# Kernel tuning notes

Hardware: AMD Instinct MI355X
Metric: run time of the kernel (lower is better)

The kernel has to match this reference:

```python
import jax, jax.numpy as jnp
import numpy as np

HIDDEN = 1024
HEADS = 16
HEAD = HIDDEN // HEADS


def setup_inputs() -> dict:
    key = jax.random.key(0)
    ks = jax.random.split(key, 10)
    s = 1.0 / np.sqrt(HIDDEN)
    inp = {
        "x": jax.random.normal(ks[0], (2, 2048, HIDDEN), dtype=jnp.float32),
        "Wq": jax.random.uniform(ks[1], (HIDDEN, HIDDEN), jnp.float32, -s, s),
        "bq": jnp.zeros((HIDDEN,), jnp.float32),
        "Wk": jax.random.uniform(ks[2], (HIDDEN, HIDDEN), jnp.float32, -s, s),
        "bk": jnp.zeros((HIDDEN,), jnp.float32),
        "Wv": jax.random.uniform(ks[3], (HIDDEN, HIDDEN), jnp.float32, -s, s),
        "bv": jnp.zeros((HIDDEN,), jnp.float32),
        "Wo": jax.random.uniform(ks[4], (HIDDEN, HIDDEN), jnp.float32, -s, s),
        "bo": jnp.zeros((HIDDEN,), jnp.float32),
        "ln_g": jnp.ones((HIDDEN,), jnp.float32),
        "ln_b": jnp.zeros((HIDDEN,), jnp.float32),
    }
    return inp


def reference(x, Wq, bq, Wk, bk, Wv, bv, Wo, bo, ln_g, ln_b):
    B, S, H = x.shape
    # pre-LN (eps=1e-5 like torch LayerNorm)
    mu = jnp.mean(x, axis=-1, keepdims=True)
    var = jnp.mean(jnp.square(x - mu), axis=-1, keepdims=True)
    xn = (x - mu) * jax.lax.rsqrt(var + 1e-5) * ln_g + ln_b
    # QKV projections (torch Linear: x @ W.T + b) -> [B,S,heads,head]
    q = (xn @ Wq.T + bq).reshape(B, S, HEADS, HEAD)
    k = (xn @ Wk.T + bk).reshape(B, S, HEADS, HEAD)
    v = (xn @ Wv.T + bv).reshape(B, S, HEADS, HEAD)
    # scaled dot-product attention, naive full scores [B,heads,S,S]
    scores = jnp.einsum("bqhd,bkhd->bhqk", q, k) / jnp.sqrt(jnp.float32(HEAD))
    attn = jax.nn.softmax(scores, axis=-1)
    ctx = jnp.einsum("bhqk,bkhd->bqhd", attn, v).reshape(B, S, H)
    out = ctx @ Wo.T + bo
    return x + out  # dropout is identity in eval
```

## Files before the change

kernel.cpp:

```cpp
#include <hip/hip_runtime.h>
#include <hip/hip_bf16.h>
#include <stdint.h>

#define HID 1024
#define SEQ 2048
#define BATCH 2
#define NHEADS 16
#define HEADDIM 64
#define MROWS (BATCH*SEQ)

#define GAS __attribute__((address_space(1)))
#define LAS __attribute__((address_space(3)))

typedef __attribute__((ext_vector_type(8))) __bf16 bf16x8;
typedef __attribute__((ext_vector_type(4))) float f32x4;

__device__ __forceinline__ ushort f2bf(float f) {
  union { float f; uint32_t u; } v; v.f = f;
  return (ushort)((v.u + 0x7FFFu + ((v.u >> 16) & 1u)) >> 16);
}

__device__ __forceinline__ void gl_lds16(const void* g, void* l) {
  __builtin_amdgcn_global_load_lds((const GAS void*)g, (LAS void*)l, 16, 0, 0);
}

__global__ __launch_bounds__(256) void k_cvt(const float* __restrict__ Wq,
                                             const float* __restrict__ Wk,
                                             const float* __restrict__ Wv,
                                             const float* __restrict__ Wo,
                                             ushort* __restrict__ dst) {
  int mat = blockIdx.y;
  const float* src = (mat == 0) ? Wq : (mat == 1) ? Wk : (mat == 2) ? Wv : Wo;
  int off = (blockIdx.x * 256 + threadIdx.x) * 4;
  float4 v = *(const float4*)(src + off);
  ushort4 o;
  o.x = f2bf(v.x); o.y = f2bf(v.y); o.z = f2bf(v.z); o.w = f2bf(v.w);
  *(ushort4*)(dst + (size_t)mat * (HID * HID) + off) = o;
}

__global__ __launch_bounds__(256) void k_ln(const float* __restrict__ x,
                                            const float* __restrict__ g,
                                            const float* __restrict__ b,
                                            ushort* __restrict__ xn) {
  int row = blockIdx.x;
  int t = threadIdx.x;
  const float* xr = x + (size_t)row * HID;
  float4 v = *(const float4*)(xr + t * 4);
  float s = v.x + v.y + v.z + v.w;
  float s2 = v.x * v.x + v.y * v.y + v.z * v.z + v.w * v.w;
  for (int m = 1; m < 64; m <<= 1) { s += __shfl_xor(s, m); s2 += __shfl_xor(s2, m); }
  __shared__ float ws[4], ws2[4];
  int wid = t >> 6;
  if ((t & 63) == 0) { ws[wid] = s; ws2[wid] = s2; }
  __syncthreads();
  s = ws[0] + ws[1] + ws[2] + ws[3];
  s2 = ws2[0] + ws2[1] + ws2[2] + ws2[3];
  float mu = s * (1.0f / HID);
  float var = s2 * (1.0f / HID) - mu * mu;
  float rstd = rsqrtf(var + 1e-5f);
  float4 gg = *(const float4*)(g + t * 4);
  float4 bb = *(const float4*)(b + t * 4);
  ushort4 o;
  o.x = f2bf((v.x - mu) * rstd * gg.x + bb.x);
  o.y = f2bf((v.y - mu) * rstd * gg.y + bb.y);
  o.z = f2bf((v.z - mu) * rstd * gg.z + bb.z);
  o.w = f2bf((v.w - mu) * rstd * gg.w + bb.w);
  *(ushort4*)(xn + (size_t)row * HID + t * 4) = o;
}

__global__ __launch_bounds__(256) void k_qkv(const ushort* __restrict__ xn,
                                             const ushort* __restrict__ wmat,
                                             const float* __restrict__ bq,
                                             const float* __restrict__ bk,
                                             const float* __restrict__ bv,
                                             ushort* __restrict__ qo,
                                             ushort* __restrict__ ko,
                                             ushort* __restrict__ vo) {
  __shared__ ushort As[128 * 32];
  __shared__ ushort Bs[128 * 32];
  int tid = threadIdx.x;
  int lane = tid & 63;
  int wv = tid >> 6;
  int quad = lane >> 4;
  int l16 = lane & 15;
  int m0 = blockIdx.x * 128;
  int ng = blockIdx.y * 128;
  int mat = ng >> 10;
  int nloc = ng & 1023;
  const ushort* wptr = wmat + (size_t)mat * (HID * HID) + (size_t)nloc * HID;
  const float* bias = (mat == 0) ? bq : (mat == 1) ? bk : bv;
  ushort* outp = (mat == 0) ? qo : (mat == 1) ? ko : vo;
  const float scl = (mat == 0) ? 0.18033688011112042f : 1.0f;

  int arow = tid >> 2;
  int acol = (tid & 3) * 8;
  int wm = (wv >> 1) * 64, wn = (wv & 1) * 64;

  f32x4 acc[4][4] = {};
  for (int k0 = 0; k0 < HID; k0 += 32) {
    __syncthreads();
    for (int t = 0; t < 2; t++) {
      gl_lds16(xn + (size_t)(m0 + t * 64 + arow) * HID + k0 + acol,
               As + t * 2048 + wv * 512);
      gl_lds16(wptr + (size_t)(t * 64 + arow) * HID + k0 + acol,
               Bs + t * 2048 + wv * 512);
    }
    __syncthreads();
    bf16x8 af[4], bfr[4];
    for (int i = 0; i < 4; i++)
      af[i] = *(const bf16x8*)&As[(wm + i * 16 + l16) * 32 + quad * 8];
    for (int n = 0; n < 4; n++)
      bfr[n] = *(const bf16x8*)&Bs[(wn + n * 16 + l16) * 32 + quad * 8];
    for (int i = 0; i < 4; i++)
      for (int n = 0; n < 4; n++)
        acc[i][n] = __builtin_amdgcn_mfma_f32_16x16x32_bf16(af[i], bfr[n], acc[i][n], 0, 0, 0);
  }
  float bv4[4];
  for (int n = 0; n < 4; n++) bv4[n] = bias[nloc + wn + n * 16 + l16];
  for (int i = 0; i < 4; i++) {
    int mrow = m0 + wm + i * 16 + quad * 4;
    for (int n = 0; n < 4; n++) {
      int col = nloc + wn + n * 16 + l16;
      int h = col >> 6, d = col & 63;
      for (int r = 0; r < 4; r++) {
        int m = mrow + r;
        int bidx = m >> 11, sidx = m & 2047;
        size_t dst = (((size_t)(bidx * NHEADS + h) * SEQ) + sidx) * HEADDIM + d;
        outp[dst] = f2bf((acc[i][n][r] + bv4[n]) * scl);
      }
    }
  }
}

__global__ __launch_bounds__(256, 2) void k_attn(const ushort* __restrict__ Q,
                                                 const ushort* __restrict__ K,
                                                 const ushort* __restrict__ V,
                                                 ushort* __restrict__ ctx) {
  __shared__ ushort Ksm[64 * 72];
  __shared__ ushort Vsm[64 * 72];
  __shared__ ushort Psm[4 * 32 * 72];
  int tid = threadIdx.x, lane = tid & 63, wv = tid >> 6, quad = lane >> 4, l16 = lane & 15;
  int bh = blockIdx.y;
  int q0 = blockIdx.x * 128;
  const ushort* Qb = Q + ((size_t)bh * SEQ + q0 + wv * 32) * HEADDIM;
  const ushort* Kb = K + (size_t)bh * SEQ * HEADDIM;
  const ushort* Vb = V + (size_t)bh * SEQ * HEADDIM;
  ushort* Pw = Psm + wv * 32 * 72;

  bf16x8 qf[2][2];
  for (int m = 0; m < 2; m++)
    for (int c = 0; c < 2; c++)
      qf[m][c] = *(const bf16x8*)(Qb + (size_t)(m * 16 + l16) * HEADDIM + c * 32 + quad * 8);

  bf16x8 ones;
  for (int j = 0; j < 8; j++) ones[j] = (__bf16)1.0f;

  f32x4 Oa[2][4] = {};
  f32x4 Os[2] = {};

  for (int kt = 0; kt < SEQ / 64; kt++) {
    const ushort* Kt = Kb + (size_t)kt * 64 * HEADDIM;
    const ushort* Vt = Vb + (size_t)kt * 64 * HEADDIM;
    __syncthreads();
    for (int it = 0; it < 2; it++) {
      int u = tid + it * 256;
      int key = u >> 3, c8 = (u & 7) * 8;
      *(int4*)&Ksm[key * 72 + c8] = *(const int4*)(Kt + key * HEADDIM + c8);
      int vkey = u & 63, vd = (u >> 6) * 8;
      int4 vvv = *(const int4*)(Vt + vkey * HEADDIM + vd);
      ushort* vp = (ushort*)&vvv;
      for (int j = 0; j < 8; j++) Vsm[(vd + j) * 72 + vkey] = vp[j];
    }
    __syncthreads();

    f32x4 sacc[2][4] = {};
    for (int nt = 0; nt < 4; nt++) {
      int krow = 2 * l16 + (nt & 1) + 32 * (nt >> 1);
      for (int c = 0; c < 2; c++) {
        bf16x8 kf = *(const bf16x8*)&Ksm[krow * 72 + c * 32 + quad * 8];
        sacc[0][nt] = __builtin_amdgcn_mfma_f32_16x16x32_bf16(qf[0][c], kf, sacc[0][nt], 0, 0, 0);
        sacc[1][nt] = __builtin_amdgcn_mfma_f32_16x16x32_bf16(qf[1][c], kf, sacc[1][nt], 0, 0, 0);
      }
    }

    for (int m = 0; m < 2; m++) {
      for (int r = 0; r < 4; r++) {
        union { float f; uint32_t u; } p0, p1, p2, p3;
        p0.f = __builtin_amdgcn_exp2f(fminf(sacc[m][0][r], 80.f));
        p1.f = __builtin_amdgcn_exp2f(fminf(sacc[m][1][r], 80.f));
        p2.f = __builtin_amdgcn_exp2f(fminf(sacc[m][2][r], 80.f));
        p3.f = __builtin_amdgcn_exp2f(fminf(sacc[m][3][r], 80.f));
        uint32_t pk01 = __builtin_amdgcn_perm(p1.u, p0.u, 0x07060302u);
        uint32_t pk23 = __builtin_amdgcn_perm(p3.u, p2.u, 0x07060302u);
        int row = m * 16 + quad * 4 + r;
        *(uint32_t*)&Pw[row * 72 + 2 * l16] = pk01;
        *(uint32_t*)&Pw[row * 72 + 32 + 2 * l16] = pk23;
      }
    }

    for (int c = 0; c < 2; c++) {
      bf16x8 pf0 = *(const bf16x8*)&Pw[(l16) * 72 + c * 32 + quad * 8];
      bf16x8 pf1 = *(const bf16x8*)&Pw[(16 + l16) * 72 + c * 32 + quad * 8];
      Os[0] = __builtin_amdgcn_mfma_f32_16x16x32_bf16(pf0, ones, Os[0], 0, 0, 0);
      Os[1] = __builtin_amdgcn_mfma_f32_16x16x32_bf16(pf1, ones, Os[1], 0, 0, 0);
      for (int nt = 0; nt < 4; nt++) {
        bf16x8 vf = *(const bf16x8*)&Vsm[(nt * 16 + l16) * 72 + c * 32 + quad * 8];
        Oa[0][nt] = __builtin_amdgcn_mfma_f32_16x16x32_bf16(pf0, vf, Oa[0][nt], 0, 0, 0);
        Oa[1][nt] = __builtin_amdgcn_mfma_f32_16x16x32_bf16(pf1, vf, Oa[1][nt], 0, 0, 0);
      }
    }
  }

  int bidx = bh >> 4, h = bh & 15;
  for (int m = 0; m < 2; m++) {
    for (int r = 0; r < 4; r++) {
      float inv = 1.0f / Os[m][r];
      int sidx = q0 + wv * 32 + m * 16 + quad * 4 + r;
      size_t base = ((size_t)(bidx * SEQ) + sidx) * HID + h * HEADDIM;
      for (int nt = 0; nt < 4; nt++)
        ctx[base + nt * 16 + l16] = f2bf(Oa[m][nt][r] * inv);
    }
  }
}

__global__ __launch_bounds__(256) void k_oproj(const ushort* __restrict__ ctx,
                                               const ushort* __restrict__ wmat,
                                               const float* __restrict__ bo,
                                               const float* __restrict__ x,
                                               float* __restrict__ out) {
  __shared__ ushort As[128 * 32];
  __shared__ ushort Bs[128 * 32];
  int tid = threadIdx.x;
  int lane = tid & 63;
  int wv = tid >> 6;
  int quad = lane >> 4;
  int l16 = lane & 15;
  int m0 = blockIdx.x * 128;
  int n0 = blockIdx.y * 128;
  const ushort* wptr = wmat + (size_t)3 * (HID * HID) + (size_t)n0 * HID;
  int arow = tid >> 2;
  int acol = (tid & 3) * 8;
  int wm = (wv >> 1) * 64, wn = (wv & 1) * 64;

  f32x4 acc[4][4] = {};
  for (int k0 = 0; k0 < HID; k0 += 32) {
    __syncthreads();
    for (int t = 0; t < 2; t++) {
      gl_lds16(ctx + (size_t)(m0 + t * 64 + arow) * HID + k0 + acol,
               As + t * 2048 + wv * 512);
      gl_lds16(wptr + (size_t)(t * 64 + arow) * HID + k0 + acol,
               Bs + t * 2048 + wv * 512);
    }
    __syncthreads();
    bf16x8 af[4], bfr[4];
    for (int i = 0; i < 4; i++)
      af[i] = *(const bf16x8*)&As[(wm + i * 16 + l16) * 32 + quad * 8];
    for (int n = 0; n < 4; n++)
      bfr[n] = *(const bf16x8*)&Bs[(wn + n * 16 + l16) * 32 + quad * 8];
    for (int i = 0; i < 4; i++)
      for (int n = 0; n < 4; n++)
        acc[i][n] = __builtin_amdgcn_mfma_f32_16x16x32_bf16(af[i], bfr[n], acc[i][n], 0, 0, 0);
  }
  float bv4[4];
  for (int n = 0; n < 4; n++) bv4[n] = bo[n0 + wn + n * 16 + l16];
  for (int i = 0; i < 4; i++) {
    int mrow = m0 + wm + i * 16 + quad * 4;
    for (int n = 0; n < 4; n++) {
      int col = n0 + wn + n * 16 + l16;
      for (int r = 0; r < 4; r++) {
        size_t idx = (size_t)(mrow + r) * HID + col;
        out[idx] = acc[i][n][r] + bv4[n] + x[idx];
      }
    }
  }
}

extern "C" void kernel_launch(void* const* d_in, const int* in_sizes, int n_in,
                              void* d_out, int out_size, void* d_ws, size_t ws_size,
                              hipStream_t stream) {
  const float* x    = (const float*)d_in[0];
  const float* Wq   = (const float*)d_in[1];
  const float* bq   = (const float*)d_in[2];
  const float* Wk   = (const float*)d_in[3];
  const float* bk   = (const float*)d_in[4];
  const float* Wv   = (const float*)d_in[5];
  const float* bv   = (const float*)d_in[6];
  const float* Wo   = (const float*)d_in[7];
  const float* bo   = (const float*)d_in[8];
  const float* ln_g = (const float*)d_in[9];
  const float* ln_b = (const float*)d_in[10];
  float* out = (float*)d_out;

  const size_t MB = 1024 * 1024;
  ushort* ws_w = (ushort*)d_ws;
  ushort* xn   = (ushort*)((char*)d_ws + 8 * MB);
  ushort* Qw   = (ushort*)((char*)d_ws + 16 * MB);
  ushort* Kw   = (ushort*)((char*)d_ws + 24 * MB);
  ushort* Vw   = (ushort*)((char*)d_ws + 32 * MB);
  ushort* Cw   = (ushort*)((char*)d_ws + 40 * MB);

  k_cvt<<<dim3(1024, 4), 256, 0, stream>>>(Wq, Wk, Wv, Wo, ws_w);
  k_ln<<<dim3(MROWS), 256, 0, stream>>>(x, ln_g, ln_b, xn);
  k_qkv<<<dim3(32, 24), 256, 0, stream>>>(xn, ws_w, bq, bk, bv, Qw, Kw, Vw);
  k_attn<<<dim3(SEQ / 128, BATCH * NHEADS), 256, 0, stream>>>(Qw, Kw, Vw, Cw);
  k_oproj<<<dim3(32, 8), 256, 0, stream>>>(Cw, ws_w, bo, x, out);
}
```

Baseline: 224.8 us.

## Double-buffer K/V tiles via async global-to-LDS loads with pre-transposed V

```diff
diff --git a/kernel.cpp b/kernel.cpp
--- a/kernel.cpp
+++ b/kernel.cpp
@@ -14,6 +14,7 @@
 
 typedef __attribute__((ext_vector_type(8))) __bf16 bf16x8;
 typedef __attribute__((ext_vector_type(4))) float f32x4;
+typedef __attribute__((ext_vector_type(2))) uint32_t u32x2;
 
 __device__ __forceinline__ ushort f2bf(float f) {
   union { float f; uint32_t u; } v; v.f = f;
@@ -125,7 +126,11 @@
       for (int r = 0; r < 4; r++) {
         int m = mrow + r;
         int bidx = m >> 11, sidx = m & 2047;
-        size_t dst = (((size_t)(bidx * NHEADS + h) * SEQ) + sidx) * HEADDIM + d;
+        size_t dst;
+        if (mat == 2)
+          dst = (((size_t)(bidx * NHEADS + h) * HEADDIM) + d) * SEQ + sidx;
+        else
+          dst = (((size_t)(bidx * NHEADS + h) * SEQ) + sidx) * HEADDIM + d;
         outp[dst] = f2bf((acc[i][n][r] + bv4[n]) * scl);
       }
     }
@@ -134,18 +139,18 @@
 
 __global__ __launch_bounds__(256, 2) void k_attn(const ushort* __restrict__ Q,
                                                  const ushort* __restrict__ K,
-                                                 const ushort* __restrict__ V,
+                                                 const ushort* __restrict__ Vt,
                                                  ushort* __restrict__ ctx) {
-  __shared__ ushort Ksm[64 * 72];
-  __shared__ ushort Vsm[64 * 72];
-  __shared__ ushort Psm[4 * 32 * 72];
+  __shared__ ushort Ksm[2][64 * 64];
+  __shared__ ushort Vsm[2][64 * 64];
+  __shared__ ushort Psm[4][32 * 64];
   int tid = threadIdx.x, lane = tid & 63, wv = tid >> 6, quad = lane >> 4, l16 = lane & 15;
   int bh = blockIdx.y;
   int q0 = blockIdx.x * 128;
   const ushort* Qb = Q + ((size_t)bh * SEQ + q0 + wv * 32) * HEADDIM;
   const ushort* Kb = K + (size_t)bh * SEQ * HEADDIM;
-  const ushort* Vb = V + (size_t)bh * SEQ * HEADDIM;
-  ushort* Pw = Psm + wv * 32 * 72;
+  const ushort* Vb = Vt + (size_t)bh * HEADDIM * SEQ;
+  ushort* Pw = Psm[wv];
 
   bf16x8 qf[2][2];
   for (int m = 0; m < 2; m++)
@@ -155,29 +160,44 @@
   bf16x8 ones;
   for (int j = 0; j < 8; j++) ones[j] = (__bf16)1.0f;
 
+  int gsl = lane & 7;
+  int rowA = wv * 8 + (lane >> 3);
+  int rowB = 32 + wv * 8 + (lane >> 3);
+  const ushort* kSrcA = Kb + rowA * HEADDIM + ((gsl ^ ((rowA >> 2) & 7)) * 8);
+  const ushort* kSrcB = Kb + rowB * HEADDIM + ((gsl ^ ((rowB >> 2) & 7)) * 8);
+  const ushort* vSrcA = Vb + (size_t)rowA * SEQ + ((gsl ^ (rowA & 7)) * 8);
+  const ushort* vSrcB = Vb + (size_t)rowB * SEQ + ((gsl ^ (rowB & 7)) * 8);
+  int ldsA = wv * 512;
+  int ldsB = 2048 + wv * 512;
+
   f32x4 Oa[2][4] = {};
   f32x4 Os[2] = {};
+  int fk = l16 & 7;
+
+  gl_lds16(kSrcA, &Ksm[0][ldsA]);
+  gl_lds16(kSrcB, &Ksm[0][ldsB]);
+  gl_lds16(vSrcA, &Vsm[0][ldsA]);
+  gl_lds16(vSrcB, &Vsm[0][ldsB]);
+  __syncthreads();
 
   for (int kt = 0; kt < SEQ / 64; kt++) {
-    const ushort* Kt = Kb + (size_t)kt * 64 * HEADDIM;
-    const ushort* Vt = Vb + (size_t)kt * 64 * HEADDIM;
-    __syncthreads();
-    for (int it = 0; it < 2; it++) {
-      int u = tid + it * 256;
-      int key = u >> 3, c8 = (u & 7) * 8;
-      *(int4*)&Ksm[key * 72 + c8] = *(const int4*)(Kt + key * HEADDIM + c8);
-      int vkey = u & 63, vd = (u >> 6) * 8;
-      int4 vvv = *(const int4*)(Vt + vkey * HEADDIM + vd);
-      ushort* vp = (ushort*)&vvv;
-      for (int j = 0; j < 8; j++) Vsm[(vd + j) * 72 + vkey] = vp[j];
-    }
-    __syncthreads();
+    int buf = kt & 1;
+    if (kt + 1 < SEQ / 64) {
+      int nb = buf ^ 1;
+      size_t ko = (size_t)(kt + 1) * 64 * HEADDIM;
+      size_t vo = (size_t)(kt + 1) * 64;
+      gl_lds16(kSrcA + ko, &Ksm[nb][ldsA]);
+      gl_lds16(kSrcB + ko, &Ksm[nb][ldsB]);
+      gl_lds16(vSrcA + vo, &Vsm[nb][ldsA]);
+      gl_lds16(vSrcB + vo, &Vsm[nb][ldsB]);
+    }
 
     f32x4 sacc[2][4] = {};
     for (int nt = 0; nt < 4; nt++) {
-      int krow = 2 * l16 + (nt & 1) + 32 * (nt >> 1);
+      int krow = 4 * l16 + nt;
       for (int c = 0; c < 2; c++) {
-        bf16x8 kf = *(const bf16x8*)&Ksm[krow * 72 + c * 32 + quad * 8];
+        int kb = c * 4 + quad;
+        bf16x8 kf = *(const bf16x8*)&Ksm[buf][krow * 64 + ((kb ^ fk) * 8)];
         sacc[0][nt] = __builtin_amdgcn_mfma_f32_16x16x32_bf16(qf[0][c], kf, sacc[0][nt], 0, 0, 0);
         sacc[1][nt] = __builtin_amdgcn_mfma_f32_16x16x32_bf16(qf[1][c], kf, sacc[1][nt], 0, 0, 0);
       }
@@ -193,22 +213,25 @@
         uint32_t pk01 = __builtin_amdgcn_perm(p1.u, p0.u, 0x07060302u);
         uint32_t pk23 = __builtin_amdgcn_perm(p3.u, p2.u, 0x07060302u);
         int row = m * 16 + quad * 4 + r;
-        *(uint32_t*)&Pw[row * 72 + 2 * l16] = pk01;
-        *(uint32_t*)&Pw[row * 72 + 32 + 2 * l16] = pk23;
+        int idx = (row * 8 + ((l16 >> 1) ^ (row & 7))) * 8 + (l16 & 1) * 4;
+        *(u32x2*)&Pw[idx] = (u32x2){pk01, pk23};
       }
     }
 
     for (int c = 0; c < 2; c++) {
-      bf16x8 pf0 = *(const bf16x8*)&Pw[(l16) * 72 + c * 32 + quad * 8];
-      bf16x8 pf1 = *(const bf16x8*)&Pw[(16 + l16) * 72 + c * 32 + quad * 8];
+      int kb = c * 4 + quad;
+      bf16x8 pf0 = *(const bf16x8*)&Pw[(l16 * 8 + (kb ^ fk)) * 8];
+      bf16x8 pf1 = *(const bf16x8*)&Pw[((16 + l16) * 8 + (kb ^ fk)) * 8];
       Os[0] = __builtin_amdgcn_mfma_f32_16x16x32_bf16(pf0, ones, Os[0], 0, 0, 0);
       Os[1] = __builtin_amdgcn_mfma_f32_16x16x32_bf16(pf1, ones, Os[1], 0, 0, 0);
       for (int nt = 0; nt < 4; nt++) {
-        bf16x8 vf = *(const bf16x8*)&Vsm[(nt * 16 + l16) * 72 + c * 32 + quad * 8];
+        int d = nt * 16 + l16;
+        bf16x8 vf = *(const bf16x8*)&Vsm[buf][d * 64 + ((kb ^ fk) * 8)];
         Oa[0][nt] = __builtin_amdgcn_mfma_f32_16x16x32_bf16(pf0, vf, Oa[0][nt], 0, 0, 0);
         Oa[1][nt] = __builtin_amdgcn_mfma_f32_16x16x32_bf16(pf1, vf, Oa[1][nt], 0, 0, 0);
       }
     }
+    __syncthreads();
   }
 
   int bidx = bh >> 4, h = bh & 15;
```

Result: faster. 210.4 us (-6.4%).
